# Performance work log

Hardware: AMD Instinct MI355X
Metric: run time of the kernel (lower is better)

The kernel has to match this reference:

```python
import jax, jax.numpy as jnp
import numpy as np

TAU = 2.0
V_THRESHOLD = 1.0
V_RESET = 0.0
TIME_STEPS = 16
SG_ALPHA = 4.0  # spikingjelly surrogate.Sigmoid default alpha


@jax.custom_vjp
def spike_fn(x):
    # heaviside forward, sigmoid surrogate backward (spikingjelly default)
    return (x >= 0.0).astype(x.dtype)

def _spike_fwd(x):
    return spike_fn(x), x

def _spike_bwd(x, g):
    s = jax.nn.sigmoid(SG_ALPHA * x)
    return (g * SG_ALPHA * s * (1.0 - s),)

spike_fn.defvjp(_spike_fwd, _spike_bwd)


def setup_inputs() -> dict:
    key = jax.random.key(0)
    k1, k2, k3 = jax.random.split(key, 3)
    B, D_in, D_h = 32768, 512, 512
    bound = 1.0 / np.sqrt(D_in)
    x = jax.random.normal(k1, (B, D_in), dtype=jnp.float32)
    W = jax.random.uniform(k2, (D_h, D_in), dtype=jnp.float32, minval=-bound, maxval=bound)
    b = jax.random.uniform(k3, (D_h,), dtype=jnp.float32, minval=-bound, maxval=bound)
    return {"x": x, "W": W, "b": b}


def reference(x, W, b):
    # fc(x) is identical every timestep in the original loop; compute once.
    cur = jnp.dot(x, W.T) + b  # [B, H]

    v0 = jnp.full_like(cur, V_RESET)
    acc0 = jnp.zeros_like(cur)

    def step(carry, _):
        v, acc = carry
        # LIF charge (decay_input=True): v = v + (x - (v - v_reset)) / tau
        v = v + (cur - (v - V_RESET)) / TAU
        spk = spike_fn(v - V_THRESHOLD)
        # hard reset, detach_reset=True
        spk_d = jax.lax.stop_gradient(spk)
        v = (1.0 - spk_d) * v + spk_d * V_RESET
        return (v, acc + spk), None

    (v, acc), _ = jax.lax.scan(step, (v0, acc0), None, length=TIME_STEPS)
    return acc / TIME_STEPS
```

## Files before the change

### kernel.cpp

```cpp
#include <hip/hip_runtime.h>


typedef float v2f __attribute__((ext_vector_type(2)));
typedef float v4f __attribute__((ext_vector_type(4)));

#define BM 128
#define BN 128
#define BK 16
#define LDA (BM + 4)
#define LDB (BN + 4)

__global__ __launch_bounds__(256)
void lif_gemm_f32(const float* __restrict__ x,
                  const float* __restrict__ W,
                  const float* __restrict__ bias,
                  float* __restrict__ out,
                  int K, int H)
{
    __shared__ __align__(16) float As[BK][LDA];
    __shared__ __align__(16) float Bs[BK][LDB];

    const int tid = threadIdx.x;
    const int tm  = tid & 15;
    const int tn  = tid >> 4;
    const int n0  = blockIdx.x * BN;
    const int m0  = blockIdx.y * BM;

    const int ra = tid >> 1;
    const int kc = (tid & 1) << 3;

    const float* xg = x + (size_t)(m0 + ra) * K + kc;
    const float* wg = W + (size_t)(n0 + ra) * K + kc;

    v2f acc[8][4];
#pragma unroll
    for (int i = 0; i < 8; ++i)
#pragma unroll
        for (int j = 0; j < 4; ++j)
            acc[i][j] = (v2f){0.0f, 0.0f};

    v4f a0 = *(const v4f*)(xg);
    v4f a1 = *(const v4f*)(xg + 4);
    v4f b0 = *(const v4f*)(wg);
    v4f b1 = *(const v4f*)(wg + 4);

    for (int k0 = 0; k0 < K; k0 += BK) {
        __syncthreads();

#pragma unroll
        for (int i = 0; i < 4; ++i) {
            As[kc + i][ra]     = a0[i];
            As[kc + 4 + i][ra] = a1[i];
            Bs[kc + i][ra]     = b0[i];
            Bs[kc + 4 + i][ra] = b1[i];
        }
        __syncthreads();

        const int kn = (k0 + BK < K) ? (k0 + BK) : k0;
        a0 = *(const v4f*)(xg + kn);
        a1 = *(const v4f*)(xg + kn + 4);
        b0 = *(const v4f*)(wg + kn);
        b1 = *(const v4f*)(wg + kn + 4);

#pragma unroll
        for (int k = 0; k < BK; ++k) {
            const v4f alo = *(const v4f*)&As[k][tm * 4];
            const v4f ahi = *(const v4f*)&As[k][64 + tm * 4];
            const v4f blo = *(const v4f*)&Bs[k][tn * 4];
            const v4f bhi = *(const v4f*)&Bs[k][64 + tn * 4];

            const v2f bb[4] = { (v2f){blo[0], blo[1]}, (v2f){blo[2], blo[3]},
                                (v2f){bhi[0], bhi[1]}, (v2f){bhi[2], bhi[3]} };
            const float av[8] = { alo[0], alo[1], alo[2], alo[3],
                                  ahi[0], ahi[1], ahi[2], ahi[3] };
#pragma unroll
            for (int i = 0; i < 8; ++i) {
                const v2f a2 = (v2f){av[i], av[i]};
#pragma unroll
                for (int j = 0; j < 4; ++j)
                    acc[i][j] = __builtin_elementwise_fma(a2, bb[j], acc[i][j]);
            }
        }
    }

    float bcol[8];
#pragma unroll
    for (int j = 0; j < 8; ++j) {
        const int col = (j < 4) ? (tn * 4 + j) : (64 + tn * 4 + (j - 4));
        bcol[j] = bias[n0 + col];
    }

#pragma unroll
    for (int i = 0; i < 8; ++i) {
        const int row = m0 + ((i < 4) ? (tm * 4 + i) : (64 + tm * 4 + (i - 4)));
        float res[8];
#pragma unroll
        for (int j = 0; j < 8; ++j) {
            const float cur = acc[i >= 4 ? i : i][j >> 1][j & 1] + bcol[j];
            float v = 0.0f;
            int cnt = 0;
#pragma unroll
            for (int t = 0; t < 16; ++t) {
                v = v + (cur - v) * 0.5f;
                const bool s = (v >= 1.0f);
                cnt += s ? 1 : 0;
                v = s ? 0.0f : v;
            }
            res[j] = (float)cnt * 0.0625f;
        }
        float* op = out + (size_t)row * H + n0;
        *(v4f*)(op + tn * 4)      = (v4f){res[0], res[1], res[2], res[3]};
        *(v4f*)(op + 64 + tn * 4) = (v4f){res[4], res[5], res[6], res[7]};
    }
}

extern "C" void kernel_launch(void* const* d_in, const int* in_sizes, int n_in,
                              void* d_out, int out_size, void* d_ws, size_t ws_size,
                              hipStream_t stream) {
    const float* x    = (const float*)d_in[0];
    const float* W    = (const float*)d_in[1];
    const float* bias = (const float*)d_in[2];
    float* out = (float*)d_out;

    const int K = 512;
    const int H = 512;
    const int B = in_sizes[0] / K;

    dim3 grid(H / BN, B / BM);
    dim3 block(256);
    lif_gemm_f32<<<grid, block, 0, stream>>>(x, W, bias, out, K, H);
}
```

Baseline: 308.0 us.

## Enlarge M tile to 256 with 512 threads and double-buffered LDS

Doubles the block tile along M to 256 rows and uses 512 threads, each still computing an 8x8 output tile. Double-buffers the shared-memory A/B tiles so only one barrier per K step is needed. Replaces the packed v2f FMAs with scalar fmaf. The aim is more reuse of each loaded W tile and less synchronisation, at the cost of more LDS per block and a possible loss of packed-FMA throughput if the compiler does not re-pack the scalar ops.

```diff
diff --git a/kernel.cpp b/kernel.cpp
--- a/kernel.cpp
+++ b/kernel.cpp
@@ -1,58 +1,59 @@
 #include <hip/hip_runtime.h>
 
 
-typedef float v2f __attribute__((ext_vector_type(2)));
 typedef float v4f __attribute__((ext_vector_type(4)));
 
-#define BM 128
+#define BM 256
 #define BN 128
 #define BK 16
 #define LDA (BM + 4)
 #define LDB (BN + 4)
 
-__global__ __launch_bounds__(256)
+__global__ __launch_bounds__(512, 4)
 void lif_gemm_f32(const float* __restrict__ x,
                   const float* __restrict__ W,
                   const float* __restrict__ bias,
                   float* __restrict__ out,
                   int K, int H)
 {
-    __shared__ __align__(16) float As[BK][LDA];
-    __shared__ __align__(16) float Bs[BK][LDB];
+    __shared__ __align__(16) float As[2][BK][LDA];
+    __shared__ __align__(16) float Bs[2][BK][LDB];
 
     const int tid = threadIdx.x;
-    const int tm  = tid & 15;
-    const int tn  = tid >> 4;
+    const int tn  = tid & 15;
+    const int tmi = tid >> 4;
     const int n0  = blockIdx.x * BN;
     const int m0  = blockIdx.y * BM;
 
     const int ra = tid >> 1;
     const int kc = (tid & 1) << 3;
+    const int rb = tid >> 2;
+    const int kb = (tid & 3) << 2;
 
     const float* xg = x + (size_t)(m0 + ra) * K + kc;
-    const float* wg = W + (size_t)(n0 + ra) * K + kc;
+    const float* wg = W + (size_t)(n0 + rb) * K + kb;
 
-    v2f acc[8][4];
+    float acc[8][8];
 #pragma unroll
     for (int i = 0; i < 8; ++i)
 #pragma unroll
-        for (int j = 0; j < 4; ++j)
-            acc[i][j] = (v2f){0.0f, 0.0f};
+        for (int j = 0; j < 8; ++j)
+            acc[i][j] = 0.0f;
 
     v4f a0 = *(const v4f*)(xg);
     v4f a1 = *(const v4f*)(xg + 4);
     v4f b0 = *(const v4f*)(wg);
-    v4f b1 = *(const v4f*)(wg + 4);
 
+    int pp = 0;
     for (int k0 = 0; k0 < K; k0 += BK) {
-        __syncthreads();
+        float (*Asp)[LDA] = As[pp];
+        float (*Bsp)[LDB] = Bs[pp];
 
 #pragma unroll
         for (int i = 0; i < 4; ++i) {
-            As[kc + i][ra]     = a0[i];
-            As[kc + 4 + i][ra] = a1[i];
-            Bs[kc + i][ra]     = b0[i];
-            Bs[kc + 4 + i][ra] = b1[i];
+            Asp[kc + i][ra]     = a0[i];
+            Asp[kc + 4 + i][ra] = a1[i];
+            Bsp[kb + i][rb]     = b0[i];
         }
         __syncthreads();
 
@@ -60,27 +61,25 @@
         a0 = *(const v4f*)(xg + kn);
         a1 = *(const v4f*)(xg + kn + 4);
         b0 = *(const v4f*)(wg + kn);
-        b1 = *(const v4f*)(wg + kn + 4);
 
 #pragma unroll
         for (int k = 0; k < BK; ++k) {
-            const v4f alo = *(const v4f*)&As[k][tm * 4];
-            const v4f ahi = *(const v4f*)&As[k][64 + tm * 4];
-            const v4f blo = *(const v4f*)&Bs[k][tn * 4];
-            const v4f bhi = *(const v4f*)&Bs[k][64 + tn * 4];
+            const v4f af0 = *(const v4f*)&Asp[k][tmi * 4];
+            const v4f af1 = *(const v4f*)&Asp[k][128 + tmi * 4];
+            const v4f blo = *(const v4f*)&Bsp[k][tn * 4];
+            const v4f bhi = *(const v4f*)&Bsp[k][64 + tn * 4];
 
-            const v2f bb[4] = { (v2f){blo[0], blo[1]}, (v2f){blo[2], blo[3]},
-                                (v2f){bhi[0], bhi[1]}, (v2f){bhi[2], bhi[3]} };
-            const float av[8] = { alo[0], alo[1], alo[2], alo[3],
-                                  ahi[0], ahi[1], ahi[2], ahi[3] };
 #pragma unroll
             for (int i = 0; i < 8; ++i) {
-                const v2f a2 = (v2f){av[i], av[i]};
+                const float a = (i < 4) ? af0[i] : af1[i - 4];
 #pragma unroll
-                for (int j = 0; j < 4; ++j)
-                    acc[i][j] = __builtin_elementwise_fma(a2, bb[j], acc[i][j]);
+                for (int j = 0; j < 8; ++j) {
+                    const float b = (j < 4) ? blo[j] : bhi[j - 4];
+                    acc[i][j] = fmaf(a, b, acc[i][j]);
+                }
             }
         }
+        pp ^= 1;
     }
 
     float bcol[8];
@@ -92,11 +91,11 @@
 
 #pragma unroll
     for (int i = 0; i < 8; ++i) {
-        const int row = m0 + ((i < 4) ? (tm * 4 + i) : (64 + tm * 4 + (i - 4)));
+        const int row = m0 + ((i < 4) ? (tmi * 4 + i) : (128 + tmi * 4 + (i - 4)));
         float res[8];
 #pragma unroll
         for (int j = 0; j < 8; ++j) {
-            const float cur = acc[i >= 4 ? i : i][j >> 1][j & 1] + bcol[j];
+            const float cur = acc[i][j] + bcol[j];
             float v = 0.0f;
             int cnt = 0;
 #pragma unroll
@@ -127,6 +126,6 @@
     const int B = in_sizes[0] / K;
 
     dim3 grid(H / BN, B / BM);
-    dim3 block(256);
+    dim3 block(512);
     lif_gemm_f32<<<grid, block, 0, stream>>>(x, W, bias, out, K, H);
 }
```

After: 313.3 us. About the same (+1.7%).
